# Performance work log

Hardware: AMD Instinct MI355X
Metric: run time of the kernel (lower is better)

## Reference

```python
import jax, jax.numpy as jnp
import numpy as np

D_MODEL = 1024
D_STATE = 16
D_CONV = 4
EXPAND = 2
NUM_LAYERS = 2
SEQ = 1024
BATCH = 2
D_INNER = EXPAND * D_MODEL          # 2048
DT_RANK = (D_MODEL + 15) // 16      # 64 (math.ceil(d_model/16))


def setup_inputs() -> dict:
    key = jax.random.key(0)
    ks = jax.random.split(key, 10)
    s = 0.02
    # A initialized as in mamba_ssm: A = repeat(arange(1, d_state+1), d_inner) -> A_log = log(A)
    A_log = jnp.log(jnp.broadcast_to(
        jnp.arange(1, D_STATE + 1, dtype=jnp.float32), (NUM_LAYERS, D_INNER, D_STATE)))
    return {
        "pe": jax.random.normal(ks[0], (SEQ, D_MODEL), jnp.float32) * s,
        "condition": jax.random.normal(ks[1], (BATCH, SEQ, D_MODEL), jnp.float32),
        "W_in": jax.random.normal(ks[2], (NUM_LAYERS, 2 * D_INNER, D_MODEL), jnp.float32) * s,
        "conv_w": jax.random.normal(ks[3], (NUM_LAYERS, D_INNER, D_CONV), jnp.float32) * s,
        "conv_b": jnp.zeros((NUM_LAYERS, D_INNER), jnp.float32),
        "W_x": jax.random.normal(ks[4], (NUM_LAYERS, DT_RANK + 2 * D_STATE, D_INNER), jnp.float32) * s,
        "W_dt": jax.random.normal(ks[5], (NUM_LAYERS, D_INNER, DT_RANK), jnp.float32) * s,
        "b_dt": jax.random.normal(ks[6], (NUM_LAYERS, D_INNER), jnp.float32) * s,
        "A_log": A_log,
        "Dp": jnp.ones((NUM_LAYERS, D_INNER), jnp.float32),
        "W_out": jax.random.normal(ks[7], (NUM_LAYERS, D_MODEL, D_INNER), jnp.float32) * s,
        "output_shape": BATCH,
    }


def _mamba_block(x, W_in, conv_w, conv_b, W_x, W_dt, b_dt, A_log, Dp, W_out):
    # x: [B, L, d_model]
    B, L, _ = x.shape
    xz = jnp.einsum('bld,ed->ble', x, W_in)          # [B, L, 2*d_inner]
    u, z = jnp.split(xz, 2, axis=-1)                 # each [B, L, d_inner]
    # causal depthwise conv1d (padding=d_conv-1, truncate to L)
    xp = jnp.pad(u, ((0, 0), (D_CONV - 1, 0), (0, 0)))
    xc = conv_b + sum(conv_w[:, k] * xp[:, k:k + L, :] for k in range(D_CONV))
    xc = jax.nn.silu(xc)                             # [B, L, d_inner]
    x_dbl = jnp.einsum('bld,ed->ble', xc, W_x)       # [B, L, dt_rank + 2*d_state]
    dt, Bm, Cm = jnp.split(x_dbl, [DT_RANK, DT_RANK + D_STATE], axis=-1)
    delta = jax.nn.softplus(jnp.einsum('blr,dr->bld', dt, W_dt) + b_dt)  # [B, L, d_inner]
    A = -jnp.exp(A_log)                              # [d_inner, d_state]

    def step(h, inputs):
        u_t, d_t, B_t, C_t = inputs                  # [B,di],[B,di],[B,ds],[B,ds]
        dA = jnp.exp(d_t[:, :, None] * A)            # [B, di, ds]
        h = dA * h + (d_t * u_t)[:, :, None] * B_t[:, None, :]
        y = jnp.einsum('bds,bs->bd', h, C_t)
        return h, y

    h0 = jnp.zeros((B, D_INNER, D_STATE), x.dtype)
    xs = (xc.transpose(1, 0, 2), delta.transpose(1, 0, 2),
          Bm.transpose(1, 0, 2), Cm.transpose(1, 0, 2))
    _, ys = jax.lax.scan(step, h0, xs)               # ys: [L, B, d_inner]
    y = ys.transpose(1, 0, 2) + xc * Dp
    out = y * jax.nn.silu(z)
    return jnp.einsum('bld,ed->ble', out, W_out)     # [B, L, d_model]


def reference(pe, condition, W_in, conv_w, conv_b, W_x, W_dt, b_dt, A_log, Dp, W_out, output_shape):
    # pe.repeat(B,1,1) + condition
    x = pe[None, :, :] + condition
    for i in range(NUM_LAYERS):
        x = _mamba_block(x, W_in[i], conv_w[i], conv_b[i], W_x[i],
                         W_dt[i], b_dt[i], A_log[i], Dp[i], W_out[i])
    return x
```

## Files before the change

### kernel.cpp

```cpp
#include <hip/hip_runtime.h>
#include <math.h>

#define D_MODEL 1024
#define D_INNER 2048
#define D_STATE 16
#define DT_RANK 64
#define SEQ 1024
#define BATCH 2
#define NLAYERS 2
#define ROWS (BATCH*SEQ)
#define XDIM 96
#define XZLD (2*D_INNER)

#define NC 32
#define CL 32
#define SDB 256

#define G2_ROWS 64
#define G2_KC 128
#define G2_BK 32
#define G2_KS (D_INNER / G2_KC)

typedef short bf16x8 __attribute__((ext_vector_type(8)));
typedef float f32x4  __attribute__((ext_vector_type(4)));

__device__ __forceinline__ unsigned short f2bf(float f) {
    union { float f; unsigned int u; } v; v.f = f;
    unsigned int u = v.u;
    return (unsigned short)((u + 0x7FFFu + ((u >> 16) & 1u)) >> 16);
}
__device__ __forceinline__ float bf2f(unsigned short u) {
    union { unsigned int i; float f; } v; v.i = ((unsigned int)u) << 16; return v.f;
}

__device__ __forceinline__ void gload_lds16(const void* g, void* s) {
    __builtin_amdgcn_global_load_lds((const __attribute__((address_space(1))) void*)g,
                                     (__attribute__((address_space(3))) void*)s, 16, 0, 0);
}

__global__ __launch_bounds__(256) void add_pe_kernel(const float* __restrict__ pe,
    const float* __restrict__ cond, float* __restrict__ X)
{
    int i = blockIdx.x * 256 + threadIdx.x;
    int total = ROWS * D_MODEL / 4;
    if (i >= total) return;
    int row  = i / (D_MODEL / 4);
    int l    = row & (SEQ - 1);
    int col4 = i - row * (D_MODEL / 4);
    float4 p = reinterpret_cast<const float4*>(pe)[l * (D_MODEL / 4) + col4];
    float4 c = reinterpret_cast<const float4*>(cond)[i];
    float4 r; r.x = p.x + c.x; r.y = p.y + c.y; r.z = p.z + c.z; r.w = p.w + c.w;
    reinterpret_cast<float4*>(X)[i] = r;
}

__global__ __launch_bounds__(256) void add_pe_kernel2(const float* __restrict__ pe,
    const float* __restrict__ cond, float* __restrict__ X, unsigned short* __restrict__ Xbf)
{
    int i = blockIdx.x * 256 + threadIdx.x;
    int total = ROWS * D_MODEL / 4;
    if (i >= total) return;
    int row  = i / (D_MODEL / 4);
    int l    = row & (SEQ - 1);
    int col4 = i - row * (D_MODEL / 4);
    float4 p = reinterpret_cast<const float4*>(pe)[l * (D_MODEL / 4) + col4];
    float4 c = reinterpret_cast<const float4*>(cond)[i];
    float4 r; r.x = p.x + c.x; r.y = p.y + c.y; r.z = p.z + c.z; r.w = p.w + c.w;
    reinterpret_cast<float4*>(X)[i] = r;
    ushort4 o; o.x = f2bf(r.x); o.y = f2bf(r.y); o.z = f2bf(r.z); o.w = f2bf(r.w);
    reinterpret_cast<ushort4*>(Xbf)[i] = o;
}

__global__ __launch_bounds__(256) void conv_bf16_dense(const float* __restrict__ src,
    unsigned short* __restrict__ dst, int n4)
{
    int i = blockIdx.x * 256 + threadIdx.x;
    if (i >= n4) return;
    float4 v = reinterpret_cast<const float4*>(src)[i];
    ushort4 o; o.x = f2bf(v.x); o.y = f2bf(v.y); o.z = f2bf(v.z); o.w = f2bf(v.w);
    reinterpret_cast<ushort4*>(dst)[i] = o;
}

__global__ __launch_bounds__(256) void conv_bf16_strided(const float* __restrict__ src,
    int ld, int cols, unsigned short* __restrict__ dst, int total4)
{
    int i = blockIdx.x * 256 + threadIdx.x;
    if (i >= total4) return;
    int c4  = cols / 4;
    int row = i / c4;
    int col = (i - row * c4) * 4;
    float4 v = *reinterpret_cast<const float4*>(src + (size_t)row * ld + col);
    ushort4 o; o.x = f2bf(v.x); o.y = f2bf(v.y); o.z = f2bf(v.z); o.w = f2bf(v.w);
    *reinterpret_cast<ushort4*>(dst + (size_t)row * cols + col) = o;
}

__global__ __launch_bounds__(256) void conv_bf16_dtcols(const float* __restrict__ XDBL,
    unsigned short* __restrict__ dst)
{
    int i = blockIdx.x * 256 + threadIdx.x;
    if (i >= ROWS * DT_RANK / 4) return;
    int m  = i >> 4;
    int c4 = (i & 15) * 4;
    float4 v = *reinterpret_cast<const float4*>(XDBL + (size_t)m * XDIM + c4);
    ushort4 o; o.x = f2bf(v.x); o.y = f2bf(v.y); o.z = f2bf(v.z); o.w = f2bf(v.w);
    *reinterpret_cast<ushort4*>(dst + (size_t)m * DT_RANK + c4) = o;
}

#define GBM 128
#define GBN 128
#define GBK 64
__global__ __launch_bounds__(256) void gemm_bf16_nt(const unsigned short* __restrict__ A,
    const unsigned short* __restrict__ B, float* __restrict__ C,
    int M, int N, int K, int ldc, const float* __restrict__ bias, int epilogue)
{
    __shared__ unsigned short As[GBM * GBK];
    __shared__ unsigned short Bs[GBN * GBK];
    int tid = threadIdx.x;
    int w = tid >> 6, l = tid & 63;
    int wr = w >> 1, wc = w & 1;
    int m0 = blockIdx.y * GBM, n0 = blockIdx.x * GBN;

    f32x4 acc[4][4];
    #pragma unroll
    for (int m = 0; m < 4; ++m)
        #pragma unroll
        for (int n = 0; n < 4; ++n) acc[m][n] = (f32x4){0.f, 0.f, 0.f, 0.f};

    int fr = l & 15, fq = l >> 4;

    for (int k0 = 0; k0 < K; k0 += GBK) {
        #pragma unroll
        for (int i = 0; i < 4; ++i) {
            int off = w * 4096 + i * 1024 + l * 16;
            int row = off >> 7;
            int col = (off & 127) >> 1;
            gload_lds16(A + (size_t)(m0 + row) * K + k0 + col,
                        (char*)As + w * 4096 + i * 1024);
        }
        #pragma unroll
        for (int i = 0; i < 4; ++i) {
            int off = w * 4096 + i * 1024 + l * 16;
            int row = off >> 7;
            int col = (off & 127) >> 1;
            gload_lds16(B + (size_t)(n0 + row) * K + k0 + col,
                        (char*)Bs + w * 4096 + i * 1024);
        }
        __syncthreads();
        #pragma unroll
        for (int kk = 0; kk < 2; ++kk) {
            bf16x8 af[4], bfr[4];
            #pragma unroll
            for (int m = 0; m < 4; ++m)
                af[m] = *(const bf16x8*)&As[(wr * 64 + m * 16 + fr) * GBK + kk * 32 + fq * 8];
            #pragma unroll
            for (int n = 0; n < 4; ++n)
                bfr[n] = *(const bf16x8*)&Bs[(wc * 64 + n * 16 + fr) * GBK + kk * 32 + fq * 8];
            #pragma unroll
            for (int m = 0; m < 4; ++m)
                #pragma unroll
                for (int n = 0; n < 4; ++n)
                    acc[m][n] = __builtin_amdgcn_mfma_f32_16x16x32_bf16(af[m], bfr[n], acc[m][n], 0, 0, 0);
        }
        __syncthreads();
    }

    #pragma unroll
    for (int m = 0; m < 4; ++m)
        #pragma unroll
        for (int n = 0; n < 4; ++n) {
            int col = n0 + wc * 64 + n * 16 + fr;
            #pragma unroll
            for (int j = 0; j < 4; ++j) {
                int row = m0 + wr * 64 + m * 16 + fq * 4 + j;
                float v = acc[m][n][j];
                if (epilogue == 1) {
                    v += bias[col];
                    v = fmaxf(v, 0.f) + log1pf(__expf(-fabsf(v)));
                }
                C[(size_t)row * ldc + col] = v;
            }
        }
}

__global__ __launch_bounds__(256) void gemm_bf16_sp_bfout(const unsigned short* __restrict__ A,
    const unsigned short* __restrict__ B, unsigned short* __restrict__ C,
    int M, int N, int K, int ldc, const float* __restrict__ bias)
{
    __shared__ unsigned short As[GBM * GBK];
    __shared__ unsigned short Bs[GBN * GBK];
    int tid = threadIdx.x;
    int w = tid >> 6, l = tid & 63;
    int wr = w >> 1, wc = w & 1;
    int m0 = blockIdx.y * GBM, n0 = blockIdx.x * GBN;

    f32x4 acc[4][4];
    #pragma unroll
    for (int m = 0; m < 4; ++m)
        #pragma unroll
        for (int n = 0; n < 4; ++n) acc[m][n] = (f32x4){0.f, 0.f, 0.f, 0.f};

    int fr = l & 15, fq = l >> 4;

    for (int k0 = 0; k0 < K; k0 += GBK) {
        #pragma unroll
        for (int i = 0; i < 4; ++i) {
            int off = w * 4096 + i * 1024 + l * 16;
            int row = off >> 7;
            int col = (off & 127) >> 1;
            gload_lds16(A + (size_t)(m0 + row) * K + k0 + col,
                        (char*)As + w * 4096 + i * 1024);
        }
        #pragma unroll
        for (int i = 0; i < 4; ++i) {
            int off = w * 4096 + i * 1024 + l * 16;
            int row = off >> 7;
            int col = (off & 127) >> 1;
            gload_lds16(B + (size_t)(n0 + row) * K + k0 + col,
                        (char*)Bs + w * 4096 + i * 1024);
        }
        __syncthreads();
        #pragma unroll
        for (int kk = 0; kk < 2; ++kk) {
            bf16x8 af[4], bfr[4];
            #pragma unroll
            for (int m = 0; m < 4; ++m)
                af[m] = *(const bf16x8*)&As[(wr * 64 + m * 16 + fr) * GBK + kk * 32 + fq * 8];
            #pragma unroll
            for (int n = 0; n < 4; ++n)
                bfr[n] = *(const bf16x8*)&Bs[(wc * 64 + n * 16 + fr) * GBK + kk * 32 + fq * 8];
            #pragma unroll
            for (int m = 0; m < 4; ++m)
                #pragma unroll
                for (int n = 0; n < 4; ++n)
                    acc[m][n] = __builtin_amdgcn_mfma_f32_16x16x32_bf16(af[m], bfr[n], acc[m][n], 0, 0, 0);
        }
        __syncthreads();
    }

    #pragma unroll
    for (int m = 0; m < 4; ++m)
        #pragma unroll
        for (int n = 0; n < 4; ++n) {
            int col = n0 + wc * 64 + n * 16 + fr;
            float bv = bias[col];
            #pragma unroll
            for (int j = 0; j < 4; ++j) {
                int row = m0 + wr * 64 + m * 16 + fq * 4 + j;
                float v = acc[m][n][j] + bv;
                v = fmaxf(v, 0.f) + log1pf(__expf(-fabsf(v)));
                C[(size_t)row * ldc + col] = f2bf(v);
            }
        }
}

__global__ __launch_bounds__(256) void gemm_bf16_nt_ks(const unsigned short* __restrict__ A, int lda,
    const unsigned short* __restrict__ B, int ldb, float* __restrict__ P,
    int M, int N, int Kper)
{
    __shared__ unsigned short As[GBM * GBK];
    __shared__ unsigned short Bs[GBN * GBK];
    int tid = threadIdx.x;
    int w = tid >> 6, l = tid & 63;
    int wr = w >> 1, wc = w & 1;
    int m0 = blockIdx.y * GBM, n0 = blockIdx.x * GBN;
    int koff = blockIdx.z * Kper;
    float* Pz = P + (size_t)blockIdx.z * M * N;

    f32x4 acc[4][4];
    #pragma unroll
    for (int m = 0; m < 4; ++m)
        #pragma unroll
        for (int n = 0; n < 4; ++n) acc[m][n] = (f32x4){0.f, 0.f, 0.f, 0.f};

    int fr = l & 15, fq = l >> 4;

    for (int k0 = 0; k0 < Kper; k0 += GBK) {
        #pragma unroll
        for (int i = 0; i < 4; ++i) {
            int off = w * 4096 + i * 1024 + l * 16;
            int row = off >> 7;
            int col = (off & 127) >> 1;
            gload_lds16(A + (size_t)(m0 + row) * lda + koff + k0 + col,
                        (char*)As + w * 4096 + i * 1024);
        }
        #pragma unroll
        for (int i = 0; i < 4; ++i) {
            int off = w * 4096 + i * 1024 + l * 16;
            int row = off >> 7;
            int col = (off & 127) >> 1;
            gload_lds16(B + (size_t)(n0 + row) * ldb + koff + k0 + col,
                        (char*)Bs + w * 4096 + i * 1024);
        }
        __syncthreads();
        #pragma unroll
        for (int kk = 0; kk < 2; ++kk) {
            bf16x8 af[4], bfr[4];
            #pragma unroll
            for (int m = 0; m < 4; ++m)
                af[m] = *(const bf16x8*)&As[(wr * 64 + m * 16 + fr) * GBK + kk * 32 + fq * 8];
            #pragma unroll
            for (int n = 0; n < 4; ++n)
                bfr[n] = *(const bf16x8*)&Bs[(wc * 64 + n * 16 + fr) * GBK + kk * 32 + fq * 8];
            #pragma unroll
            for (int m = 0; m < 4; ++m)
                #pragma unroll
                for (int n = 0; n < 4; ++n)
                    acc[m][n] = __builtin_amdgcn_mfma_f32_16x16x32_bf16(af[m], bfr[n], acc[m][n], 0, 0, 0);
        }
        __syncthreads();
    }

    #pragma unroll
    for (int m = 0; m < 4; ++m)
        #pragma unroll
        for (int n = 0; n < 4; ++n) {
            int col = n0 + wc * 64 + n * 16 + fr;
            #pragma unroll
            for (int j = 0; j < 4; ++j) {
                int row = m0 + wr * 64 + m * 16 + fq * 4 + j;
                Pz[(size_t)row * N + col] = acc[m][n][j];
            }
        }
}

__global__ __launch_bounds__(256) void gemm4_reduce(const float* __restrict__ P,
    float* __restrict__ X, unsigned short* __restrict__ Xbf)
{
    int i = blockIdx.x * 256 + threadIdx.x;
    if (i >= ROWS * D_MODEL / 4) return;
    float4 a = reinterpret_cast<const float4*>(P)[i];
    float4 b = reinterpret_cast<const float4*>(P + (size_t)ROWS * D_MODEL)[i];
    float4 r; r.x = a.x + b.x; r.y = a.y + b.y; r.z = a.z + b.z; r.w = a.w + b.w;
    reinterpret_cast<float4*>(X)[i] = r;
    ushort4 o; o.x = f2bf(r.x); o.y = f2bf(r.y); o.z = f2bf(r.z); o.w = f2bf(r.w);
    reinterpret_cast<ushort4*>(Xbf)[i] = o;
}

__global__ __launch_bounds__(256) void gemm2_splitk(const float* __restrict__ A,
    const float* __restrict__ B, float* __restrict__ P)
{
    __shared__ float As[G2_BK][G2_ROWS];
    __shared__ float Bs[G2_BK][XDIM + 1];
    int tid = threadIdx.x;
    int m0 = blockIdx.x * G2_ROWS;
    int kc = blockIdx.y;
    int k0 = kc * G2_KC;

    int rg = tid >> 4;
    int cg = tid & 15;
    float acc[4][6];
    #pragma unroll
    for (int i = 0; i < 4; ++i)
        #pragma unroll
        for (int j = 0; j < 6; ++j) acc[i][j] = 0.f;

    for (int kb = 0; kb < G2_KC; kb += G2_BK) {
        {
            int row = tid & 63;
            int kk  = (tid >> 6) * 4;
            #pragma unroll
            for (int i = 0; i < 2; ++i) {
                float4 v = *(const float4*)(A + (size_t)(m0 + row) * D_INNER + k0 + kb + kk + i * 16);
                As[kk + i * 16 + 0][row] = v.x;
                As[kk + i * 16 + 1][row] = v.y;
                As[kk + i * 16 + 2][row] = v.z;
                As[kk + i * 16 + 3][row] = v.w;
            }
        }
// ... 133 lines not shown
__global__ __launch_bounds__(256) void conv_silu_kernel(const float* __restrict__ XZ,
    const float* __restrict__ cw, const float* __restrict__ cb, float* __restrict__ XC)
{
    int idx = blockIdx.x * 256 + threadIdx.x;
    if (idx >= ROWS * (D_INNER / 4)) return;
    int d4   = idx % (D_INNER / 4);
    int rl   = idx / (D_INNER / 4);
    int l    = rl & (SEQ - 1);
    int base = rl - l;
    int d    = d4 * 4;

    float4 acc = reinterpret_cast<const float4*>(cb)[d4];
    float w[4][4];
    #pragma unroll
    for (int dd = 0; dd < 4; ++dd) {
        float4 wv = *reinterpret_cast<const float4*>(cw + (size_t)(d + dd) * 4);
        w[dd][0] = wv.x; w[dd][1] = wv.y; w[dd][2] = wv.z; w[dd][3] = wv.w;
    }
    #pragma unroll
    for (int k = 0; k < 4; ++k) {
        int lr = l - 3 + k;
        if (lr < 0) continue;
        float4 u = *reinterpret_cast<const float4*>(XZ + (size_t)(base + lr) * XZLD + d);
        acc.x += w[0][k] * u.x; acc.y += w[1][k] * u.y;
        acc.z += w[2][k] * u.z; acc.w += w[3][k] * u.w;
    }
    acc.x = acc.x / (1.f + __expf(-acc.x));
    acc.y = acc.y / (1.f + __expf(-acc.y));
    acc.z = acc.z / (1.f + __expf(-acc.z));
    acc.w = acc.w / (1.f + __expf(-acc.w));
    reinterpret_cast<float4*>(XC)[idx] = acc;
}


__global__ __launch_bounds__(SDB) void scan_part1b(const float* __restrict__ XC,
    const unsigned short* __restrict__ DL, const float* __restrict__ XDBL,
    const float* __restrict__ A_log, float* __restrict__ Psum, float* __restrict__ Ssum)
{
    __shared__ float sB[CL][16];
    int tid = threadIdx.x;
    int d = blockIdx.x * SDB + tid;
    int c = blockIdx.y, b = blockIdx.z;
    size_t r0 = (size_t)b * SEQ + (size_t)c * CL;

    if (tid < CL * 4) {
        int t = tid >> 2, j = (tid & 3) * 4;
        *(float4*)&sB[t][j] = *(const float4*)(XDBL + (r0 + t) * XDIM + DT_RANK + j);
    }

    float a[D_STATE], S[D_STATE];
    #pragma unroll
    for (int i = 0; i < 4; ++i) {
        float4 v = *(const float4*)(A_log + (size_t)d * D_STATE + i * 4);
        a[i*4+0] = -__expf(v.x); a[i*4+1] = -__expf(v.y);
        a[i*4+2] = -__expf(v.z); a[i*4+3] = -__expf(v.w);
    }
    #pragma unroll
    for (int s = 0; s < D_STATE; ++s) S[s] = 0.f;
    float sumdl = 0.f;
    __syncthreads();

    for (int t = 0; t < CL; ++t) {
        float dl = bf2f(DL[(r0 + t) * D_INNER + d]);
        float uu = XC[(r0 + t) * D_INNER + d];
        float du = dl * uu;
        sumdl += dl;
// ... 9 lines not shown
            S[s] = e * S[s] + du * bv[s];
        }
    }

    size_t o = (((size_t)b * NC + c) * D_INNER + d) * D_STATE;
    #pragma unroll
    for (int i = 0; i < 4; ++i) {
        float4 p, s4;
        p.x = __expf(a[i*4+0] * sumdl); p.y = __expf(a[i*4+1] * sumdl);
        p.z = __expf(a[i*4+2] * sumdl); p.w = __expf(a[i*4+3] * sumdl);
        s4.x = S[i*4+0]; s4.y = S[i*4+1]; s4.z = S[i*4+2]; s4.w = S[i*4+3];
        *(float4*)(Psum + o + i * 4) = p;
        *(float4*)(Ssum + o + i * 4) = s4;
    }
}

__global__ __launch_bounds__(256) void scan_prefix(float* __restrict__ Psum,
    const float* __restrict__ Ssum)
{
    int idx = blockIdx.x * 256 + threadIdx.x;
    int b = idx >> 15;
    int rem = idx & 32767;
    float h = 0.f;
    for (int c = 0; c < NC; ++c) {
        size_t o = (((size_t)b * NC + c) * D_INNER * D_STATE) + rem;
        float p = Psum[o];
        float s = Ssum[o];
        Psum[o] = h;
        h = p * h + s;
    }
}

__global__ __launch_bounds__(SDB) void scan_part2b(const float* __restrict__ XC,
    unsigned short* __restrict__ DL, const float* __restrict__ XZ,
    const float* __restrict__ XDBL, const float* __restrict__ A_log,
    const float* __restrict__ Dp, const float* __restrict__ Hin)
{
    __shared__ float sBC[CL][32];
    int tid = threadIdx.x;
    int d = blockIdx.x * SDB + tid;
    int c = blockIdx.y, b = blockIdx.z;
    size_t r0 = (size_t)b * SEQ + (size_t)c * CL;

    {
        int t = tid >> 3, j = (tid & 7) * 4;
        *(float4*)&sBC[t][j] = *(const float4*)(XDBL + (r0 + t) * XDIM + DT_RANK + j);
    }

    float a[D_STATE], h[D_STATE];
    #pragma unroll
    for (int i = 0; i < 4; ++i) {
        float4 v = *(const float4*)(A_log + (size_t)d * D_STATE + i * 4);
        a[i*4+0] = -__expf(v.x); a[i*4+1] = -__expf(v.y);
        a[i*4+2] = -__expf(v.z); a[i*4+3] = -__expf(v.w);
    }
    size_t ho = (((size_t)b * NC + c) * D_INNER + d) * D_STATE;
    #pragma unroll
    for (int i = 0; i < 4; ++i) {
        float4 v = *(const float4*)(Hin + ho + i * 4);
        h[i*4+0] = v.x; h[i*4+1] = v.y; h[i*4+2] = v.z; h[i*4+3] = v.w;
    }
    float dp = Dp[d];
    __syncthreads();

    for (int t = 0; t < CL; ++t) {
        float dl = bf2f(DL[(r0 + t) * D_INNER + d]);
        float uu = XC[(r0 + t) * D_INNER + d];
        float z  = XZ[(r0 + t) * XZLD + D_INNER + d];
        float du = dl * uu;
        float4 b0 = *(const float4*)&sBC[t][0];
        float4 b1 = *(const float4*)&sBC[t][4];
        float4 b2 = *(const float4*)&sBC[t][8];
        float4 b3 = *(const float4*)&sBC[t][12];
        float4 c0 = *(const float4*)&sBC[t][16];
        float4 c1 = *(const float4*)&sBC[t][20];
        float4 c2 = *(const float4*)&sBC[t][24];
        float4 c3 = *(const float4*)&sBC[t][28];
        float bv[16] = {b0.x,b0.y,b0.z,b0.w, b1.x,b1.y,b1.z,b1.w,
                        b2.x,b2.y,b2.z,b2.w, b3.x,b3.y,b3.z,b3.w};
        float cv[16] = {c0.x,c0.y,c0.z,c0.w, c1.x,c1.y,c1.z,c1.w,
                        c2.x,c2.y,c2.z,c2.w, c3.x,c3.y,c3.z,c3.w};
        float y = 0.f;
        #pragma unroll
        for (int s = 0; s < D_STATE; ++s) {
            float e = __expf(dl * a[s]);
            h[s] = e * h[s] + du * bv[s];
            y += h[s] * cv[s];
        }
        float sz = z / (1.f + __expf(-z));
        DL[(r0 + t) * D_INNER + d] = f2bf((y + uu * dp) * sz);
    }
}

__global__ __launch_bounds__(SDB) void scan_part1(const float* __restrict__ XC,
    const float* __restrict__ XZ, const float* __restrict__ XDBL,
    const float* __restrict__ A_log, float* __restrict__ Psum, float* __restrict__ Ssum)
{
    __shared__ float sB[CL][16];
    int tid = threadIdx.x;
    int d = blockIdx.x * SDB + tid;
    int c = blockIdx.y, b = blockIdx.z;
// ... 129 lines not shown
        float z  = XZ[r * XZLD + D_INNER + d];
        float Bv = XDBL[r * XDIM + DT_RANK + s];
        float Cv = XDBL[r * XDIM + DT_RANK + D_STATE + s];
        float e  = __expf(dl * a);
        h = e * h + dl * uu * Bv;
        float y = h * Cv;
        y += __shfl_xor(y, 1);
        y += __shfl_xor(y, 2);
        y += __shfl_xor(y, 4);
        y += __shfl_xor(y, 8);
        if (s == 0) {
            float sz = z / (1.f + __expf(-z));
            XZ[r * XZLD + d] = (y + uu * dp) * sz;
        }
    }
}

extern "C" void kernel_launch(void* const* d_in, const int* in_sizes, int n_in,
                              void* d_out, int out_size, void* d_ws, size_t ws_size,
                              hipStream_t stream)
{
    const float* pe    = (const float*)d_in[0];
    const float* cond  = (const float*)d_in[1];
    const float* W_in  = (const float*)d_in[2];
    const float* cw    = (const float*)d_in[3];
    const float* cb    = (const float*)d_in[4];
    const float* W_x   = (const float*)d_in[5];
    const float* W_dt  = (const float*)d_in[6];
    const float* b_dt  = (const float*)d_in[7];
    const float* A_log = (const float*)d_in[8];
    const float* Dp    = (const float*)d_in[9];
    const float* W_out = (const float*)d_in[10];

    float* X    = (float*)d_out;
    float* XZ   = (float*)d_ws;
    float* XC   = XZ + (size_t)ROWS * XZLD;
    float* XDBL = XC + (size_t)ROWS * D_INNER;

    unsigned short* BF0 = (unsigned short*)(XDBL + (size_t)ROWS * XDIM);
    unsigned short* BF1 = BF0 + (size_t)ROWS * D_INNER;
    float* SCR = (float*)(BF1 + (size_t)2 * D_INNER * D_MODEL);
    size_t need_A = ((size_t)ROWS * XZLD + (size_t)ROWS * D_INNER + (size_t)ROWS * XDIM) * 4
                  + ((size_t)ROWS * D_INNER + (size_t)2 * D_INNER * D_MODEL) * 2
                  + (size_t)4 * 1024 * 1024 * 4;

    void* rest = (void*)(XDBL + (size_t)ROWS * XDIM);
    unsigned short* Abf = (unsigned short*)rest;
    unsigned short* Bbf = Abf + (size_t)ROWS * D_INNER;
    float* PpartB = (float*)rest;
    float* PsumB  = (float*)rest;
    float* SsumB  = PsumB + (size_t)BATCH * NC * D_INNER * D_STATE;
    size_t need_B = ((size_t)ROWS * XZLD + (size_t)ROWS * D_INNER + (size_t)ROWS * XDIM) * 4
                  + ((size_t)ROWS * D_INNER + (size_t)ROWS * D_INNER) * 2;

    if (ws_size >= need_A) {
        unsigned short* dtbf   = BF1;
        unsigned short* Wdtbf  = BF1 + (size_t)ROWS * DT_RANK;
        float* Psum = SCR;
        float* Ssum = SCR + (size_t)BATCH * NC * D_INNER * D_STATE;

        add_pe_kernel2<<<ROWS * D_MODEL / 4 / 256, 256, 0, stream>>>(pe, cond, X, BF0);

        for (int l = 0; l < NLAYERS; ++l) {
            const float* W_in_l  = W_in  + (size_t)l * 2 * D_INNER * D_MODEL;
            const float* W_out_l = W_out + (size_t)l * D_MODEL * D_INNER;
            const float* W_x_l   = W_x   + (size_t)l * XDIM * D_INNER;
            const float* W_dt_l  = W_dt  + (size_t)l * D_INNER * DT_RANK;
            const float* b_dt_l  = b_dt  + (size_t)l * D_INNER;
            const float* A_log_l = A_log + (size_t)l * D_INNER * D_STATE;
            const float* Dp_l    = Dp    + (size_t)l * D_INNER;

            conv_bf16_dense<<<(2 * D_INNER * D_MODEL / 4 + 255) / 256, 256, 0, stream>>>(
                W_in_l, BF1, 2 * D_INNER * D_MODEL / 4);
            gemm_bf16_nt<<<dim3(2 * D_INNER / GBN, ROWS / GBM), 256, 0, stream>>>(
                BF0, BF1, XZ, ROWS, 2 * D_INNER, D_MODEL, XZLD, nullptr, 0);
            conv_silu_kernel<<<ROWS * (D_INNER / 4) / 256, 256, 0, stream>>>(
                XZ, cw + (size_t)l * D_INNER * 4, cb + (size_t)l * D_INNER, XC);
            gemm2_splitk<<<dim3(ROWS / G2_ROWS, G2_KS), 256, 0, stream>>>(XC, W_x_l, SCR);
            gemm2_reduce<<<(ROWS * XDIM / 4 + 255) / 256, 256, 0, stream>>>(SCR, XDBL, dtbf);
            conv_bf16_dense<<<(D_INNER * DT_RANK / 4 + 255) / 256, 256, 0, stream>>>(
                W_dt_l, Wdtbf, D_INNER * DT_RANK / 4);
            gemm_bf16_sp_bfout<<<dim3(D_INNER / GBN, ROWS / GBM), 256, 0, stream>>>(
                dtbf, Wdtbf, BF0, ROWS, D_INNER, DT_RANK, D_INNER, b_dt_l);
            scan_part1b<<<dim3(D_INNER / SDB, NC, BATCH), SDB, 0, stream>>>(
                XC, BF0, XDBL, A_log_l, Psum, Ssum);
            scan_prefix<<<BATCH * D_INNER * D_STATE / 256, 256, 0, stream>>>(Psum, Ssum);
            scan_part2b<<<dim3(D_INNER / SDB, NC, BATCH), SDB, 0, stream>>>(
                XC, BF0, XZ, XDBL, A_log_l, Dp_l, Psum);
            conv_bf16_dense<<<(D_MODEL * D_INNER / 4 + 255) / 256, 256, 0, stream>>>(
                W_out_l, BF1, D_MODEL * D_INNER / 4);
            gemm_bf16_nt_ks<<<dim3(D_MODEL / GBN, ROWS / GBM, 2), 256, 0, stream>>>(
                BF0, D_INNER, BF1, D_INNER, SCR, ROWS, D_MODEL, D_INNER / 2);
            gemm4_reduce<<<(ROWS * D_MODEL / 4 + 255) / 256, 256, 0, stream>>>(SCR, X, BF0);
        }
    } else if (ws_size >= need_B) {
        add_pe_kernel<<<ROWS * D_MODEL / 4 / 256, 256, 0, stream>>>(pe, cond, X);
        for (int l = 0; l < NLAYERS; ++l) {
            const float* W_in_l  = W_in  + (size_t)l * 2 * D_INNER * D_MODEL;
            const float* W_out_l = W_out + (size_t)l * D_MODEL * D_INNER;
            const float* W_x_l   = W_x   + (size_t)l * XDIM * D_INNER;
            const float* W_dt_l  = W_dt  + (size_t)l * D_INNER * DT_RANK;
            const float* b_dt_l  = b_dt  + (size_t)l * D_INNER;
            const float* A_log_l = A_log + (size_t)l * D_INNER * D_STATE;
            const float* Dp_l    = Dp    + (size_t)l * D_INNER;

            conv_bf16_dense<<<(ROWS * D_MODEL / 4 + 255) / 256, 256, 0, stream>>>(X, Abf, ROWS * D_MODEL / 4);
            conv_bf16_dense<<<(2 * D_INNER * D_MODEL / 4 + 255) / 256, 256, 0, stream>>>(W_in_l, Bbf, 2 * D_INNER * D_MODEL / 4);
            gemm_bf16_nt<<<dim3(2 * D_INNER / GBN, ROWS / GBM), 256, 0, stream>>>(
                Abf, Bbf, XZ, ROWS, 2 * D_INNER, D_MODEL, XZLD, nullptr, 0);
            conv_silu_kernel<<<ROWS * (D_INNER / 4) / 256, 256, 0, stream>>>(
                XZ, cw + (size_t)l * D_INNER * 4, cb + (size_t)l * D_INNER, XC);
            gemm2_splitk<<<dim3(ROWS / G2_ROWS, G2_KS), 256, 0, stream>>>(XC, W_x_l, PpartB);
            gemm2_reduce<<<(ROWS * XDIM / 4 + 255) / 256, 256, 0, stream>>>(PpartB, XDBL, nullptr);
            conv_bf16_dtcols<<<(ROWS * DT_RANK / 4 + 255) / 256, 256, 0, stream>>>(XDBL, Abf);
            conv_bf16_dense<<<(D_INNER * DT_RANK / 4 + 255) / 256, 256, 0, stream>>>(W_dt_l, Bbf, D_INNER * DT_RANK / 4);
            gemm_bf16_nt<<<dim3(D_INNER / GBN, ROWS / GBM), 256, 0, stream>>>(
                Abf, Bbf, XZ, ROWS, D_INNER, DT_RANK, XZLD, b_dt_l, 1);
            scan_part1<<<dim3(D_INNER / SDB, NC, BATCH), SDB, 0, stream>>>(
                XC, XZ, XDBL, A_log_l, PsumB, SsumB);
            scan_prefix<<<BATCH * D_INNER * D_STATE / 256, 256, 0, stream>>>(PsumB, SsumB);
            scan_part2<<<dim3(D_INNER / SDB, NC, BATCH), SDB, 0, stream>>>(
                XC, XZ, XDBL, A_log_l, Dp_l, PsumB);
            conv_bf16_strided<<<(ROWS * D_INNER / 4 + 255) / 256, 256, 0, stream>>>(
                XZ, XZLD, D_INNER, Abf, ROWS * D_INNER / 4);
            conv_bf16_dense<<<(D_MODEL * D_INNER / 4 + 255) / 256, 256, 0, stream>>>(W_out_l, Bbf, D_MODEL * D_INNER / 4);
            gemm_bf16_nt<<<dim3(D_MODEL / GBN, ROWS / GBM), 256, 0, stream>>>(
                Abf, Bbf, X, ROWS, D_MODEL, D_INNER, D_MODEL, nullptr, 0);
        }
    } else {
        add_pe_kernel<<<ROWS * D_MODEL / 4 / 256, 256, 0, stream>>>(pe, cond, X);
        for (int l = 0; l < NLAYERS; ++l) {
            gemm_nt<<<dim3(2 * D_INNER / BN, ROWS / BM), 256, 0, stream>>>(
                X, D_MODEL, W_in + (size_t)l * 2 * D_INNER * D_MODEL, D_MODEL,
                XZ, XZLD, ROWS, 2 * D_INNER, D_MODEL, nullptr, 0);
            conv_silu_kernel<<<ROWS * (D_INNER / 4) / 256, 256, 0, stream>>>(
                XZ, cw + (size_t)l * D_INNER * 4, cb + (size_t)l * D_INNER, XC);
            gemm_nt<<<dim3((XDIM + BN - 1) / BN, ROWS / BM), 256, 0, stream>>>(
                XC, D_INNER, W_x + (size_t)l * XDIM * D_INNER, D_INNER,
                XDBL, XDIM, ROWS, XDIM, D_INNER, nullptr, 0);
            gemm_nt<<<dim3(D_INNER / BN, ROWS / BM), 256, 0, stream>>>(
                XDBL, XDIM, W_dt + (size_t)l * D_INNER * DT_RANK, DT_RANK,
                XZ, XZLD, ROWS, D_INNER, DT_RANK, b_dt + (size_t)l * D_INNER, 1);
            scan_kernel2<<<dim3(D_INNER / 16, BATCH), 256, 0, stream>>>(
                XC, XZ, XDBL, A_log + (size_t)l * D_INNER * D_STATE, Dp + (size_t)l * D_INNER);
            gemm_nt<<<dim3(D_MODEL / BN, ROWS / BM), 256, 0, stream>>>(
                XZ, XZLD, W_out + (size_t)l * D_MODEL * D_INNER, D_INNER,
                X, D_MODEL, ROWS, D_MODEL, D_INNER, nullptr, 0);
        }
    }
}
```

Measured before the change: 394.6 us.

## Store in-proj output as bf16 and convert all weights to bf16 once up front

The in-projection GEMM now writes bf16 instead of fp32, and the conv+SiLU and scan_part2 kernels read the bf16 XZ buffer directly. All layers' W_in, W_out and W_dt are converted to bf16 in three batched launches before the layer loop instead of per layer. The fp32 X write is dropped for intermediate layers, and the workspace is laid out at fixed offsets. This cuts memory traffic and launch count at the cost of extra rounding on the z gate and conv input.

```diff
diff --git a/kernel.cpp b/kernel.cpp
--- a/kernel.cpp
+++ b/kernel.cpp
@@ -53,8 +53,8 @@
     reinterpret_cast<float4*>(X)[i] = r;
 }
 
-__global__ __launch_bounds__(256) void add_pe_kernel2(const float* __restrict__ pe,
-    const float* __restrict__ cond, float* __restrict__ X, unsigned short* __restrict__ Xbf)
+__global__ __launch_bounds__(256) void add_pe_bf(const float* __restrict__ pe,
+    const float* __restrict__ cond, unsigned short* __restrict__ Xbf)
 {
     int i = blockIdx.x * 256 + threadIdx.x;
     int total = ROWS * D_MODEL / 4;
@@ -64,9 +64,9 @@
     int col4 = i - row * (D_MODEL / 4);
     float4 p = reinterpret_cast<const float4*>(pe)[l * (D_MODEL / 4) + col4];
     float4 c = reinterpret_cast<const float4*>(cond)[i];
-    float4 r; r.x = p.x + c.x; r.y = p.y + c.y; r.z = p.z + c.z; r.w = p.w + c.w;
-    reinterpret_cast<float4*>(X)[i] = r;
-    ushort4 o; o.x = f2bf(r.x); o.y = f2bf(r.y); o.z = f2bf(r.z); o.w = f2bf(r.w);
+    ushort4 o;
+    o.x = f2bf(p.x + c.x); o.y = f2bf(p.y + c.y);
+    o.z = f2bf(p.z + c.z); o.w = f2bf(p.w + c.w);
     reinterpret_cast<ushort4*>(Xbf)[i] = o;
 }
 
@@ -108,6 +108,42 @@
 #define GBM 128
 #define GBN 128
 #define GBK 64
+
+#define GEMM_STAGE(Ap, Bp, lda, ldb, koff)                                      \
+    _Pragma("unroll")                                                           \
+    for (int i_ = 0; i_ < 4; ++i_) {                                            \
+        int off_ = w * 4096 + i_ * 1024 + l * 16;                               \
+        int row_ = off_ >> 7;                                                   \
+        int col_ = (off_ & 127) >> 1;                                           \
+        gload_lds16(Ap + (size_t)(m0 + row_) * (lda) + (koff) + col_,           \
+                    (char*)As + w * 4096 + i_ * 1024);                          \
+    }                                                                           \
+    _Pragma("unroll")                                                           \
+    for (int i_ = 0; i_ < 4; ++i_) {                                            \
+        int off_ = w * 4096 + i_ * 1024 + l * 16;                               \
+        int row_ = off_ >> 7;                                                   \
+        int col_ = (off_ & 127) >> 1;                                           \
+        gload_lds16(Bp + (size_t)(n0 + row_) * (ldb) + (koff) + col_,           \
+                    (char*)Bs + w * 4096 + i_ * 1024);                          \
+    }
+
+#define GEMM_MFMA_STEP                                                          \
+    _Pragma("unroll")                                                           \
+    for (int kk = 0; kk < 2; ++kk) {                                            \
+        bf16x8 af[4], bfr[4];                                                   \
+        _Pragma("unroll")                                                       \
+        for (int m = 0; m < 4; ++m)                                             \
+            af[m] = *(const bf16x8*)&As[(wr * 64 + m * 16 + fr) * GBK + kk * 32 + fq * 8]; \
+        _Pragma("unroll")                                                       \
+        for (int n = 0; n < 4; ++n)                                             \
+            bfr[n] = *(const bf16x8*)&Bs[(wc * 64 + n * 16 + fr) * GBK + kk * 32 + fq * 8]; \
+        _Pragma("unroll")                                                       \
+        for (int m = 0; m < 4; ++m)                                             \
+            _Pragma("unroll")                                                   \
+            for (int n = 0; n < 4; ++n)                                         \
+                acc[m][n] = __builtin_amdgcn_mfma_f32_16x16x32_bf16(af[m], bfr[n], acc[m][n], 0, 0, 0); \
+    }
+
 __global__ __launch_bounds__(256) void gemm_bf16_nt(const unsigned short* __restrict__ A,
     const unsigned short* __restrict__ B, float* __restrict__ C,
     int M, int N, int K, int ldc, const float* __restrict__ bias, int epilogue)
@@ -124,42 +160,12 @@
     for (int m = 0; m < 4; ++m)
         #pragma unroll
         for (int n = 0; n < 4; ++n) acc[m][n] = (f32x4){0.f, 0.f, 0.f, 0.f};
-
     int fr = l & 15, fq = l >> 4;
 
     for (int k0 = 0; k0 < K; k0 += GBK) {
-        #pragma unroll
-        for (int i = 0; i < 4; ++i) {
-            int off = w * 4096 + i * 1024 + l * 16;
-            int row = off >> 7;
-            int col = (off & 127) >> 1;
-            gload_lds16(A + (size_t)(m0 + row) * K + k0 + col,
-                        (char*)As + w * 4096 + i * 1024);
-        }
-        #pragma unroll
-        for (int i = 0; i < 4; ++i) {
-            int off = w * 4096 + i * 1024 + l * 16;
-            int row = off >> 7;
-            int col = (off & 127) >> 1;
-            gload_lds16(B + (size_t)(n0 + row) * K + k0 + col,
-                        (char*)Bs + w * 4096 + i * 1024);
-        }
-        __syncthreads();
-        #pragma unroll
-        for (int kk = 0; kk < 2; ++kk) {
-            bf16x8 af[4], bfr[4];
-            #pragma unroll
-            for (int m = 0; m < 4; ++m)
-                af[m] = *(const bf16x8*)&As[(wr * 64 + m * 16 + fr) * GBK + kk * 32 + fq * 8];
-            #pragma unroll
-            for (int n = 0; n < 4; ++n)
-                bfr[n] = *(const bf16x8*)&Bs[(wc * 64 + n * 16 + fr) * GBK + kk * 32 + fq * 8];
-            #pragma unroll
-            for (int m = 0; m < 4; ++m)
-                #pragma unroll
-                for (int n = 0; n < 4; ++n)
-                    acc[m][n] = __builtin_amdgcn_mfma_f32_16x16x32_bf16(af[m], bfr[n], acc[m][n], 0, 0, 0);
-        }
+        GEMM_STAGE(A, B, K, K, k0)
+        __syncthreads();
+        GEMM_MFMA_STEP
         __syncthreads();
     }
 
@@ -181,9 +187,9 @@
         }
 }
 
-__global__ __launch_bounds__(256) void gemm_bf16_sp_bfout(const unsigned short* __restrict__ A,
+__global__ __launch_bounds__(256) void gemm_bf16_nt_bfout(const unsigned short* __restrict__ A,
     const unsigned short* __restrict__ B, unsigned short* __restrict__ C,
-    int M, int N, int K, int ldc, const float* __restrict__ bias)
+    int M, int N, int K, int ldc)
 {
     __shared__ unsigned short As[GBM * GBK];
     __shared__ unsigned short Bs[GBN * GBK];
@@ -197,42 +203,50 @@
     for (int m = 0; m < 4; ++m)
         #pragma unroll
         for (int n = 0; n < 4; ++n) acc[m][n] = (f32x4){0.f, 0.f, 0.f, 0.f};
-
     int fr = l & 15, fq = l >> 4;
 
     for (int k0 = 0; k0 < K; k0 += GBK) {
-        #pragma unroll
-        for (int i = 0; i < 4; ++i) {
-            int off = w * 4096 + i * 1024 + l * 16;
-            int row = off >> 7;
-            int col = (off & 127) >> 1;
-            gload_lds16(A + (size_t)(m0 + row) * K + k0 + col,
-                        (char*)As + w * 4096 + i * 1024);
-        }
-        #pragma unroll
-        for (int i = 0; i < 4; ++i) {
-            int off = w * 4096 + i * 1024 + l * 16;
-            int row = off >> 7;
-            int col = (off & 127) >> 1;
-            gload_lds16(B + (size_t)(n0 + row) * K + k0 + col,
-                        (char*)Bs + w * 4096 + i * 1024);
-        }
-        __syncthreads();
-        #pragma unroll
-        for (int kk = 0; kk < 2; ++kk) {
-            bf16x8 af[4], bfr[4];
+        GEMM_STAGE(A, B, K, K, k0)
+        __syncthreads();
+        GEMM_MFMA_STEP
+        __syncthreads();
+    }
+
+    #pragma unroll
+    for (int m = 0; m < 4; ++m)
+        #pragma unroll
+        for (int n = 0; n < 4; ++n) {
+            int col = n0 + wc * 64 + n * 16 + fr;
             #pragma unroll
-            for (int m = 0; m < 4; ++m)
-                af[m] = *(const bf16x8*)&As[(wr * 64 + m * 16 + fr) * GBK + kk * 32 + fq * 8];
-            #pragma unroll
-            for (int n = 0; n < 4; ++n)
-                bfr[n] = *(const bf16x8*)&Bs[(wc * 64 + n * 16 + fr) * GBK + kk * 32 + fq * 8];
-            #pragma unroll
-            for (int m = 0; m < 4; ++m)
-                #pragma unroll
-                for (int n = 0; n < 4; ++n)
-                    acc[m][n] = __builtin_amdgcn_mfma_f32_16x16x32_bf16(af[m], bfr[n], acc[m][n], 0, 0, 0);
-        }
+            for (int j = 0; j < 4; ++j) {
+                int row = m0 + wr * 64 + m * 16 + fq * 4 + j;
+                C[(size_t)row * ldc + col] = f2bf(acc[m][n][j]);
+            }
+        }
+}
+
+__global__ __launch_bounds__(256) void gemm_bf16_sp_bfout(const unsigned short* __restrict__ A,
+    const unsigned short* __restrict__ B, unsigned short* __restrict__ C,
+    int M, int N, int K, int ldc, const float* __restrict__ bias)
+{
+    __shared__ unsigned short As[GBM * GBK];
+    __shared__ unsigned short Bs[GBN * GBK];
+    int tid = threadIdx.x;
+    int w = tid >> 6, l = tid & 63;
+    int wr = w >> 1, wc = w & 1;
+    int m0 = blockIdx.y * GBM, n0 = blockIdx.x * GBN;
+
+    f32x4 acc[4][4];
+    #pragma unroll
+    for (int m = 0; m < 4; ++m)
+        #pragma unroll
+        for (int n = 0; n < 4; ++n) acc[m][n] = (f32x4){0.f, 0.f, 0.f, 0.f};
+    int fr = l & 15, fq = l >> 4;
+
+    for (int k0 = 0; k0 < K; k0 += GBK) {
+        GEMM_STAGE(A, B, K, K, k0)
+        __syncthreads();
+        GEMM_MFMA_STEP
         __syncthreads();
     }
 
@@ -270,42 +284,12 @@
     for (int m = 0; m < 4; ++m)
         #pragma unroll
         for (int n = 0; n < 4; ++n) acc[m][n] = (f32x4){0.f, 0.f, 0.f, 0.f};
-
     int fr = l & 15, fq = l >> 4;
 
     for (int k0 = 0; k0 < Kper; k0 += GBK) {
-        #pragma unroll
-        for (int i = 0; i < 4; ++i) {
-            int off = w * 4096 + i * 1024 + l * 16;
-            int row = off >> 7;
-            int col = (off & 127) >> 1;
-            gload_lds16(A + (size_t)(m0 + row) * lda + koff + k0 + col,
-                        (char*)As + w * 4096 + i * 1024);
-        }
-        #pragma unroll
-        for (int i = 0; i < 4; ++i) {
-            int off = w * 4096 + i * 1024 + l * 16;
-            int row = off >> 7;
-            int col = (off & 127) >> 1;
-            gload_lds16(B + (size_t)(n0 + row) * ldb + koff + k0 + col,
-                        (char*)Bs + w * 4096 + i * 1024);
-        }
-        __syncthreads();
-        #pragma unroll
-        for (int kk = 0; kk < 2; ++kk) {
-            bf16x8 af[4], bfr[4];
-            #pragma unroll
-            for (int m = 0; m < 4; ++m)
-                af[m] = *(const bf16x8*)&As[(wr * 64 + m * 16 + fr) * GBK + kk * 32 + fq * 8];
-            #pragma unroll
-            for (int n = 0; n < 4; ++n)
-                bfr[n] = *(const bf16x8*)&Bs[(wc * 64 + n * 16 + fr) * GBK + kk * 32 + fq * 8];
-            #pragma unroll
-            for (int m = 0; m < 4; ++m)
-                #pragma unroll
-                for (int n = 0; n < 4; ++n)
-                    acc[m][n] = __builtin_amdgcn_mfma_f32_16x16x32_bf16(af[m], bfr[n], acc[m][n], 0, 0, 0);
-        }
+        GEMM_STAGE(A, B, lda, ldb, koff + k0)
+        __syncthreads();
+        GEMM_MFMA_STEP
         __syncthreads();
     }
 
@@ -330,9 +314,11 @@
     float4 a = reinterpret_cast<const float4*>(P)[i];
     float4 b = reinterpret_cast<const float4*>(P + (size_t)ROWS * D_MODEL)[i];
     float4 r; r.x = a.x + b.x; r.y = a.y + b.y; r.z = a.z + b.z; r.w = a.w + b.w;
-    reinterpret_cast<float4*>(X)[i] = r;
-    ushort4 o; o.x = f2bf(r.x); o.y = f2bf(r.y); o.z = f2bf(r.z); o.w = f2bf(r.w);
-    reinterpret_cast<ushort4*>(Xbf)[i] = o;
+    if (X) reinterpret_cast<float4*>(X)[i] = r;
+    if (Xbf) {
+        ushort4 o; o.x = f2bf(r.x); o.y = f2bf(r.y); o.z = f2bf(r.z); o.w = f2bf(r.w);
+        reinterpret_cast<ushort4*>(Xbf)[i] = o;
+    }
 }
 
 __global__ __launch_bounds__(256) void gemm2_splitk(const float* __restrict__ A,
@@ -532,6 +518,39 @@
     reinterpret_cast<float4*>(XC)[idx] = acc;
 }
 
+__global__ __launch_bounds__(256) void conv_silu_bf(const unsigned short* __restrict__ XZbf,
+    const float* __restrict__ cw, const float* __restrict__ cb, float* __restrict__ XC)
+{
+    int idx = blockIdx.x * 256 + threadIdx.x;
+    if (idx >= ROWS * (D_INNER / 4)) return;
+    int d4   = idx % (D_INNER / 4);
+    int rl   = idx / (D_INNER / 4);
+    int l    = rl & (SEQ - 1);
+    int base = rl - l;
+    int d    = d4 * 4;
+
+    float4 acc = reinterpret_cast<const float4*>(cb)[d4];
+    float w[4][4];
+    #pragma unroll
+    for (int dd = 0; dd < 4; ++dd) {
+        float4 wv = *reinterpret_cast<const float4*>(cw + (size_t)(d + dd) * 4);
+        w[dd][0] = wv.x; w[dd][1] = wv.y; w[dd][2] = wv.z; w[dd][3] = wv.w;
+    }
+    #pragma unroll
+    for (int k = 0; k < 4; ++k) {
+        int lr = l - 3 + k;
+        if (lr < 0) continue;
+        ushort4 uv = *reinterpret_cast<const ushort4*>(XZbf + (size_t)(base + lr) * XZLD + d);
+        acc.x += w[0][k] * bf2f(uv.x); acc.y += w[1][k] * bf2f(uv.y);
+        acc.z += w[2][k] * bf2f(uv.z); acc.w += w[3][k] * bf2f(uv.w);
+    }
+    acc.x = acc.x / (1.f + __expf(-acc.x));
+    acc.y = acc.y / (1.f + __expf(-acc.y));
+    acc.z = acc.z / (1.f + __expf(-acc.z));
+    acc.w = acc.w / (1.f + __expf(-acc.w));
+    reinterpret_cast<float4*>(XC)[idx] = acc;
+}
+
 
 __global__ __launch_bounds__(SDB) void scan_part1b(const float* __restrict__ XC,
     const unsigned short* __restrict__ DL, const float* __restrict__ XDBL,
@@ -607,7 +626,7 @@
 }
 
 __global__ __launch_bounds__(SDB) void scan_part2b(const float* __restrict__ XC,
-    unsigned short* __restrict__ DL, const float* __restrict__ XZ,
+    unsigned short* __restrict__ DL, const unsigned short* __restrict__ XZbf,
     const float* __restrict__ XDBL, const float* __restrict__ A_log,
     const float* __restrict__ Dp, const float* __restrict__ Hin)
 {
@@ -641,7 +660,7 @@
     for (int t = 0; t < CL; ++t) {
         float dl = bf2f(DL[(r0 + t) * D_INNER + d]);
         float uu = XC[(r0 + t) * D_INNER + d];
-        float z  = XZ[(r0 + t) * XZLD + D_INNER + d];
+        float z  = bf2f(XZbf[(r0 + t) * XZLD + D_INNER + d]);
         float du = dl * uu;
         float4 b0 = *(const float4*)&sBC[t][0];
         float4 b1 = *(const float4*)&sBC[t][4];
@@ -837,19 +856,24 @@
     const float* Dp    = (const float*)d_in[9];
     const float* W_out = (const float*)d_in[10];
 
-    float* X    = (float*)d_out;
-    float* XZ   = (float*)d_ws;
-    float* XC   = XZ + (size_t)ROWS * XZLD;
-    float* XDBL = XC + (size_t)ROWS * D_INNER;
-
-    unsigned short* BF0 = (unsigned short*)(XDBL + (size_t)ROWS * XDIM);
-    unsigned short* BF1 = BF0 + (size_t)ROWS * D_INNER;
-    float* SCR = (float*)(BF1 + (size_t)2 * D_INNER * D_MODEL);
-    size_t need_A = ((size_t)ROWS * XZLD + (size_t)ROWS * D_INNER + (size_t)ROWS * XDIM) * 4
-                  + ((size_t)ROWS * D_INNER + (size_t)2 * D_INNER * D_MODEL) * 2
-                  + (size_t)4 * 1024 * 1024 * 4;
-
-    void* rest = (void*)(XDBL + (size_t)ROWS * XDIM);
+    float* X = (float*)d_out;
+
+    char* wsp = (char*)d_ws;
+    unsigned short* XZbf = (unsigned short*)wsp;
+    float* XC    = (float*)(wsp + 16777216);
+    float* XDBL  = (float*)(wsp + 33554432);
+    unsigned short* BF0   = (unsigned short*)(wsp + 34340864);
+    unsigned short* dtbf  = (unsigned short*)(wsp + 42729472);
+    unsigned short* WINbf = (unsigned short*)(wsp + 42991616);
+    unsigned short* WOUTbf= (unsigned short*)(wsp + 59768832);
+    unsigned short* WDTbf = (unsigned short*)(wsp + 68157440);
+    float* SCR   = (float*)(wsp + 68681728);
+    size_t need_A = 68681728 + 16777216;
+
+    float* XZb   = (float*)d_ws;
+    float* XCb   = XZb + (size_t)ROWS * XZLD;
+    float* XDBLb = XCb + (size_t)ROWS * D_INNER;
+    void* rest = (void*)(XDBLb + (size_t)ROWS * XDIM);
     unsigned short* Abf = (unsigned short*)rest;
     unsigned short* Bbf = Abf + (size_t)ROWS * D_INNER;
     float* PpartB = (float*)rest;
@@ -859,44 +883,43 @@
                   + ((size_t)ROWS * D_INNER + (size_t)ROWS * D_INNER) * 2;
 
     if (ws_size >= need_A) {
-        unsigned short* dtbf   = BF1;
-        unsigned short* Wdtbf  = BF1 + (size_t)ROWS * DT_RANK;
         float* Psum = SCR;
         float* Ssum = SCR + (size_t)BATCH * NC * D_INNER * D_STATE;
 
-        add_pe_kernel2<<<ROWS * D_MODEL / 4 / 256, 256, 0, stream>>>(pe, cond, X, BF0);
+        conv_bf16_dense<<<(NLAYERS * 2 * D_INNER * D_MODEL / 4 + 255) / 256, 256, 0, stream>>>(
+            W_in, WINbf, NLAYERS * 2 * D_INNER * D_MODEL / 4);
+        conv_bf16_dense<<<(NLAYERS * D_MODEL * D_INNER / 4 + 255) / 256, 256, 0, stream>>>(
+            W_out, WOUTbf, NLAYERS * D_MODEL * D_INNER / 4);
+        conv_bf16_dense<<<(NLAYERS * D_INNER * DT_RANK / 4 + 255) / 256, 256, 0, stream>>>(
+            W_dt, WDTbf, NLAYERS * D_INNER * DT_RANK / 4);
+        add_pe_bf<<<ROWS * D_MODEL / 4 / 256, 256, 0, stream>>>(pe, cond, BF0);
 
         for (int l = 0; l < NLAYERS; ++l) {
-            const float* W_in_l  = W_in  + (size_t)l * 2 * D_INNER * D_MODEL;
-            const float* W_out_l = W_out + (size_t)l * D_MODEL * D_INNER;
+            const unsigned short* WINl  = WINbf  + (size_t)l * 2 * D_INNER * D_MODEL;
+            const unsigned short* WOUTl = WOUTbf + (size_t)l * D_MODEL * D_INNER;
+            const unsigned short* WDTl  = WDTbf  + (size_t)l * D_INNER * DT_RANK;
             const float* W_x_l   = W_x   + (size_t)l * XDIM * D_INNER;
-            const float* W_dt_l  = W_dt  + (size_t)l * D_INNER * DT_RANK;
             const float* b_dt_l  = b_dt  + (size_t)l * D_INNER;
             const float* A_log_l = A_log + (size_t)l * D_INNER * D_STATE;
             const float* Dp_l    = Dp    + (size_t)l * D_INNER;
 
-            conv_bf16_dense<<<(2 * D_INNER * D_MODEL / 4 + 255) / 256, 256, 0, stream>>>(
-                W_in_l, BF1, 2 * D_INNER * D_MODEL / 4);
-            gemm_bf16_nt<<<dim3(2 * D_INNER / GBN, ROWS / GBM), 256, 0, stream>>>(
-                BF0, BF1, XZ, ROWS, 2 * D_INNER, D_MODEL, XZLD, nullptr, 0);
-            conv_silu_kernel<<<ROWS * (D_INNER / 4) / 256, 256, 0, stream>>>(
-                XZ, cw + (size_t)l * D_INNER * 4, cb + (size_t)l * D_INNER, XC);
+            gemm_bf16_nt_bfout<<<dim3(2 * D_INNER / GBN, ROWS / GBM), 256, 0, stream>>>(
+                BF0, WINl, XZbf, ROWS, 2 * D_INNER, D_MODEL, XZLD);
+            conv_silu_bf<<<ROWS * (D_INNER / 4) / 256, 256, 0, stream>>>(
+                XZbf, cw + (size_t)l * D_INNER * 4, cb + (size_t)l * D_INNER, XC);
             gemm2_splitk<<<dim3(ROWS / G2_ROWS, G2_KS), 256, 0, stream>>>(XC, W_x_l, SCR);
             gemm2_reduce<<<(ROWS * XDIM / 4 + 255) / 256, 256, 0, stream>>>(SCR, XDBL, dtbf);
-            conv_bf16_dense<<<(D_INNER * DT_RANK / 4 + 255) / 256, 256, 0, stream>>>(
-                W_dt_l, Wdtbf, D_INNER * DT_RANK / 4);
             gemm_bf16_sp_bfout<<<dim3(D_INNER / GBN, ROWS / GBM), 256, 0, stream>>>(
-                dtbf, Wdtbf, BF0, ROWS, D_INNER, DT_RANK, D_INNER, b_dt_l);
+                dtbf, WDTl, BF0, ROWS, D_INNER, DT_RANK, D_INNER, b_dt_l);
             scan_part1b<<<dim3(D_INNER / SDB, NC, BATCH), SDB, 0, stream>>>(
                 XC, BF0, XDBL, A_log_l, Psum, Ssum);
             scan_prefix<<<BATCH * D_INNER * D_STATE / 256, 256, 0, stream>>>(Psum, Ssum);
             scan_part2b<<<dim3(D_INNER / SDB, NC, BATCH), SDB, 0, stream>>>(
-                XC, BF0, XZ, XDBL, A_log_l, Dp_l, Psum);
-            conv_bf16_dense<<<(D_MODEL * D_INNER / 4 + 255) / 256, 256, 0, stream>>>(
-                W_out_l, BF1, D_MODEL * D_INNER / 4);
+                XC, BF0, XZbf, XDBL, A_log_l, Dp_l, Psum);
             gemm_bf16_nt_ks<<<dim3(D_MODEL / GBN, ROWS / GBM, 2), 256, 0, stream>>>(
-                BF0, D_INNER, BF1, D_INNER, SCR, ROWS, D_MODEL, D_INNER / 2);
-            gemm4_reduce<<<(ROWS * D_MODEL / 4 + 255) / 256, 256, 0, stream>>>(SCR, X, BF0);
+                BF0, D_INNER, WOUTl, D_INNER, SCR, ROWS, D_MODEL, D_INNER / 2);
+            gemm4_reduce<<<(ROWS * D_MODEL / 4 + 255) / 256, 256, 0, stream>>>(
+                SCR, (l == NLAYERS - 1) ? X : nullptr, (l < NLAYERS - 1) ? BF0 : nullptr);
         }
     } else if (ws_size >= need_B) {
         add_pe_kernel<<<ROWS * D_MODEL / 4 / 256, 256, 0, stream>>>(pe, cond, X);
@@ -912,22 +935,22 @@
             conv_bf16_dense<<<(ROWS * D_MODEL / 4 + 255) / 256, 256, 0, stream>>>(X, Abf, ROWS * D_MODEL / 4);
             conv_bf16_dense<<<(2 * D_INNER * D_MODEL / 4 + 255) / 256, 256, 0, stream>>>(W_in_l, Bbf, 2 * D_INNER * D_MODEL / 4);
             gemm_bf16_nt<<<dim3(2 * D_INNER / GBN, ROWS / GBM), 256, 0, stream>>>(
-                Abf, Bbf, XZ, ROWS, 2 * D_INNER, D_MODEL, XZLD, nullptr, 0);
+                Abf, Bbf, XZb, ROWS, 2 * D_INNER, D_MODEL, XZLD, nullptr, 0);
             conv_silu_kernel<<<ROWS * (D_INNER / 4) / 256, 256, 0, stream>>>(
-                XZ, cw + (size_t)l * D_INNER * 4, cb + (size_t)l * D_INNER, XC);
-            gemm2_splitk<<<dim3(ROWS / G2_ROWS, G2_KS), 256, 0, stream>>>(XC, W_x_l, PpartB);
-            gemm2_reduce<<<(ROWS * XDIM / 4 + 255) / 256, 256, 0, stream>>>(PpartB, XDBL, nullptr);
-            conv_bf16_dtcols<<<(ROWS * DT_RANK / 4 + 255) / 256, 256, 0, stream>>>(XDBL, Abf);
+                XZb, cw + (size_t)l * D_INNER * 4, cb + (size_t)l * D_INNER, XCb);
+            gemm2_splitk<<<dim3(ROWS / G2_ROWS, G2_KS), 256, 0, stream>>>(XCb, W_x_l, PpartB);
+            gemm2_reduce<<<(ROWS * XDIM / 4 + 255) / 256, 256, 0, stream>>>(PpartB, XDBLb, nullptr);
+            conv_bf16_dtcols<<<(ROWS * DT_RANK / 4 + 255) / 256, 256, 0, stream>>>(XDBLb, Abf);
             conv_bf16_dense<<<(D_INNER * DT_RANK / 4 + 255) / 256, 256, 0, stream>>>(W_dt_l, Bbf, D_INNER * DT_RANK / 4);
             gemm_bf16_nt<<<dim3(D_INNER / GBN, ROWS / GBM), 256, 0, stream>>>(
-                Abf, Bbf, XZ, ROWS, D_INNER, DT_RANK, XZLD, b_dt_l, 1);
+                Abf, Bbf, XZb, ROWS, D_INNER, DT_RANK, XZLD, b_dt_l, 1);
             scan_part1<<<dim3(D_INNER / SDB, NC, BATCH), SDB, 0, stream>>>(
-                XC, XZ, XDBL, A_log_l, PsumB, SsumB);
+                XCb, XZb, XDBLb, A_log_l, PsumB, SsumB);
             scan_prefix<<<BATCH * D_INNER * D_STATE / 256, 256, 0, stream>>>(PsumB, SsumB);
             scan_part2<<<dim3(D_INNER / SDB, NC, BATCH), SDB, 0, stream>>>(
-                XC, XZ, XDBL, A_log_l, Dp_l, PsumB);
+                XCb, XZb, XDBLb, A_log_l, Dp_l, PsumB);
             conv_bf16_strided<<<(ROWS * D_INNER / 4 + 255) / 256, 256, 0, stream>>>(
-                XZ, XZLD, D_INNER, Abf, ROWS * D_INNER / 4);
+                XZb, XZLD, D_INNER, Abf, ROWS * D_INNER / 4);
             conv_bf16_dense<<<(D_MODEL * D_INNER / 4 + 255) / 256, 256, 0, stream>>>(W_out_l, Bbf, D_MODEL * D_INNER / 4);
             gemm_bf16_nt<<<dim3(D_MODEL / GBN, ROWS / GBM), 256, 0, stream>>>(
                 Abf, Bbf, X, ROWS, D_MODEL, D_INNER, D_MODEL, nullptr, 0);
@@ -937,19 +960,19 @@
         for (int l = 0; l < NLAYERS; ++l) {
             gemm_nt<<<dim3(2 * D_INNER / BN, ROWS / BM), 256, 0, stream>>>(
                 X, D_MODEL, W_in + (size_t)l * 2 * D_INNER * D_MODEL, D_MODEL,
-                XZ, XZLD, ROWS, 2 * D_INNER, D_MODEL, nullptr, 0);
+                XZb, XZLD, ROWS, 2 * D_INNER, D_MODEL, nullptr, 0);
             conv_silu_kernel<<<ROWS * (D_INNER / 4) / 256, 256, 0, stream>>>(
-                XZ, cw + (size_t)l * D_INNER * 4, cb + (size_t)l * D_INNER, XC);
+                XZb, cw + (size_t)l * D_INNER * 4, cb + (size_t)l * D_INNER, XCb);
             gemm_nt<<<dim3((XDIM + BN - 1) / BN, ROWS / BM), 256, 0, stream>>>(
-                XC, D_INNER, W_x + (size_t)l * XDIM * D_INNER, D_INNER,
-                XDBL, XDIM, ROWS, XDIM, D_INNER, nullptr, 0);
+                XCb, D_INNER, W_x + (size_t)l * XDIM * D_INNER, D_INNER,
+                XDBLb, XDIM, ROWS, XDIM, D_INNER, nullptr, 0);
             gemm_nt<<<dim3(D_INNER / BN, ROWS / BM), 256, 0, stream>>>(
-                XDBL, XDIM, W_dt + (size_t)l * D_INNER * DT_RANK, DT_RANK,
-                XZ, XZLD, ROWS, D_INNER, DT_RANK, b_dt + (size_t)l * D_INNER, 1);
+                XDBLb, XDIM, W_dt + (size_t)l * D_INNER * DT_RANK, DT_RANK,
+                XZb, XZLD, ROWS, D_INNER, DT_RANK, b_dt + (size_t)l * D_INNER, 1);
             scan_kernel2<<<dim3(D_INNER / 16, BATCH), 256, 0, stream>>>(
-                XC, XZ, XDBL, A_log + (size_t)l * D_INNER * D_STATE, Dp + (size_t)l * D_INNER);
+                XCb, XZb, XDBLb, A_log + (size_t)l * D_INNER * D_STATE, Dp + (size_t)l * D_INNER);
             gemm_nt<<<dim3(D_MODEL / BN, ROWS / BM), 256, 0, stream>>>(
-                XZ, XZLD, W_out + (size_t)l * D_MODEL * D_INNER, D_INNER,
+                XZb, XZLD, W_out + (size_t)l * D_MODEL * D_INNER, D_INNER,
                 X, D_MODEL, ROWS, D_MODEL, D_INNER, nullptr, 0);
         }
     }
```

After: 381.6 us. 1.03x faster.
